# Kernel optimization log

Hardware: AMD Instinct MI355X
Metric: run time of the kernel (lower is better)

Reference implementation:

```python
import math
import jax, jax.numpy as jnp
import numpy as np

N_HEADS = 16
HEAD_DIM = 128
NUM_BUCKETS = 32
MAX_DISTANCE = 128
ROPE_BASE = 10000.0


def _rope_cos_sin(seq_len, head_dim, dtype):
    inv_freq = 1.0 / (ROPE_BASE ** (jnp.arange(0, head_dim, 2, dtype=jnp.float32) / head_dim))
    ang = jnp.arange(seq_len, dtype=jnp.float32)[:, None] * inv_freq[None, :]  # [S, hd/2]
    return jnp.cos(ang).astype(dtype), jnp.sin(ang).astype(dtype)


def _apply_rope(t, cos, sin):
    # t: [B, S, H, D] (NeoX rotate-half); cos/sin: [S, D/2]
    d2 = t.shape[-1] // 2
    t1, t2 = t[..., :d2], t[..., d2:]
    c = cos[None, :, None, :]
    s = sin[None, :, None, :]
    return jnp.concatenate([t1 * c - t2 * s, t2 * c + t1 * s], axis=-1)


def _relative_bucket(q_len, k_len):
    # unidirectional (causal) T5 bucketing: relative_position = 0 - min(mem - ctx, 0)
    ctx = jnp.arange(q_len, dtype=jnp.int32)[:, None]
    mem = jnp.arange(k_len, dtype=jnp.int32)[None, :]
    n = jnp.maximum(ctx - mem, 0)  # [Q, K]
    max_exact = NUM_BUCKETS // 2
    is_small = n < max_exact
    nf = jnp.maximum(n, 1).astype(jnp.float32)
    large = (jnp.log(nf / max_exact) / math.log(MAX_DISTANCE / max_exact)
             * (NUM_BUCKETS - max_exact)).astype(jnp.int32) + max_exact
    large = jnp.minimum(large, NUM_BUCKETS - 1)
    return jnp.where(is_small, n, large)


def setup_inputs() -> dict:
    key = jax.random.key(0)
    k1, k2, k3, k4 = jax.random.split(key, 4)
    B, S, H = 2, 2048, 2048
    return {
        "x": jax.random.normal(k1, (B, S, H), jnp.float32),
        "qkv_w": jax.random.normal(k2, (H, 3 * H), jnp.float32) * 0.02,
        "dense_w": jax.random.normal(k3, (H, H), jnp.float32) * 0.02,
        "rel_attn_table": jax.random.normal(k4, (NUM_BUCKETS, N_HEADS), jnp.float32) * 0.1,
    }


def reference(x, qkv_w, dense_w, rel_attn_table):
    B, S, H = x.shape
    qkv = x @ qkv_w                         # [B, S, 3H]
    q, k, v = jnp.split(qkv, 3, axis=-1)
    q = q.reshape(B, S, N_HEADS, HEAD_DIM)
    k = k.reshape(B, S, N_HEADS, HEAD_DIM)
    v = v.reshape(B, S, N_HEADS, HEAD_DIM)

    cos, sin = _rope_cos_sin(S, HEAD_DIM, x.dtype)
    q = _apply_rope(q, cos, sin)
    k = _apply_rope(k, cos, sin)

    scale = 1.0 / math.sqrt(HEAD_DIM)       # q_scaling = 1.0
    scores = jnp.einsum("bqhd,bkhd->bhqk", q, k) * scale  # [B, nH, S, S]

    # T5 relative position bias: embedding(bucket, table).permute(2,0,1) -> [1, nH, S, S]
    bucket = _relative_bucket(S, S)
    bias = rel_attn_table[bucket]            # [S, S, nH]
    scores = scores + jnp.transpose(bias, (2, 0, 1))[None]

    # causal mask (make_causal_mask): key index > query index -> large negative
    causal = jnp.tril(jnp.ones((S, S), dtype=bool))
    neg = jnp.asarray(jnp.finfo(x.dtype).min, x.dtype)
    scores = jnp.where(causal[None, None], scores, neg)

    probs = jax.nn.softmax(scores, axis=-1)
    ctx = jnp.einsum("bhqk,bkhd->bqhd", probs, v).reshape(B, S, H)
    return ctx @ dense_w
```

## Files before the change

### kernel.cpp

```cpp
#include <hip/hip_runtime.h>

typedef unsigned short u16;
typedef __bf16 bf16_t;
typedef __bf16 bf16x8 __attribute__((ext_vector_type(8)));
typedef float f32x4 __attribute__((ext_vector_type(4)));
typedef unsigned short u16x8 __attribute__((ext_vector_type(8)));
typedef unsigned short u16x4 __attribute__((ext_vector_type(4)));

#define S_LEN 2048
#define NHEAD 16
#define HD 128
#define HID 2048
#define QKV_N 6144

__device__ __forceinline__ float b2f(u16 u) {
  union { unsigned int i; float f; } x; x.i = ((unsigned int)u) << 16; return x.f;
}
__device__ __forceinline__ u16 f2b(float f) {
  bf16_t h = (bf16_t)f;
  return __builtin_bit_cast(unsigned short, h);
}

__device__ __forceinline__ void gl_lds16(const u16* g, u16* l) {
  __builtin_amdgcn_global_load_lds(
      (const __attribute__((address_space(1))) unsigned int*)g,
      (__attribute__((address_space(3))) unsigned int*)l, 16, 0, 0);
}

__global__ void detect_dtype_k(const void* __restrict__ x, int* __restrict__ flag) {
  __shared__ int cnt;
  if (threadIdx.x == 0) cnt = 0;
  __syncthreads();
  const u16* xu = (const u16*)x;
  int sane = 0;
  for (int i = threadIdx.x; i < 8192; i += 256) {
    int e = (xu[i] >> 7) & 0xFF;
    if (e == 0 || (e > 100 && e < 140)) sane++;
  }
  atomicAdd(&cnt, sane);
  __syncthreads();
  if (threadIdx.x == 0) *flag = (cnt < 7373) ? 1 : 0;
}

__global__ __launch_bounds__(256) void convert_any_k(const void* __restrict__ in, u16* __restrict__ out,
                                                     const int* __restrict__ flag) {
  int i = (blockIdx.x * 256 + threadIdx.x) * 4;
  if (*flag) {
    const float4 v = *(const float4*)((const float*)in + i);
    u16x4 o = {f2b(v.x), f2b(v.y), f2b(v.z), f2b(v.w)};
    *(u16x4*)(out + i) = o;
  } else {
    *(u16x4*)(out + i) = *(const u16x4*)((const u16*)in + i);
  }
}

__global__ __launch_bounds__(256) void transpose_any(const void* __restrict__ in,
                                                     u16* __restrict__ out, int R, int C,
                                                     const int* __restrict__ flag) {
  __shared__ u16 t[64][65];
  bool isf = (*flag != 0);
  int tid = threadIdx.x;
  int r0 = blockIdx.y * 64, c0 = blockIdx.x * 64;
#pragma unroll
  for (int p = 0; p < 16; ++p) {
    int e = p * 256 + tid;
    int r = e >> 6, c = e & 63;
    size_t idx = (size_t)(r0 + r) * C + (c0 + c);
    t[r][c] = isf ? f2b(((const float*)in)[idx]) : ((const u16*)in)[idx];
  }
  __syncthreads();
#pragma unroll
  for (int p = 0; p < 16; ++p) {
    int e = p * 256 + tid;
    int r = e >> 6, c = e & 63;
    out[(size_t)(c0 + r) * R + (r0 + c)] = t[c][r];
  }
}

__global__ void rope_table_k(float* __restrict__ tab) {
  int i = blockIdx.x * 256 + threadIdx.x;
  int s = i >> 6, d = i & 63;
  float inv = expf(-(float)d * (9.210340371976184f / 64.0f));
  float ang = (float)s * inv;
  tab[s * 128 + d] = cosf(ang);
  tab[s * 128 + 64 + d] = sinf(ang);
}

__global__ void build_bias_k(const void* __restrict__ table, float* __restrict__ bias,
                             const int* __restrict__ flag) {
  int i = blockIdx.x * 256 + threadIdx.x;
  int h = i >> 11, dist = i & 2047;
  int bucket;
  if (dist < 16) bucket = dist;
  else {
    int lb = (int)(logf((float)dist * 0.0625f) / 2.0794415f * 16.0f) + 16;
    bucket = lb < 31 ? lb : 31;
  }
  int ti = bucket * NHEAD + h;
  float tv = (*flag) ? ((const float*)table)[ti] : b2f(((const u16*)table)[ti]);
  bias[h * 2048 + dist] = tv;
}

template <bool F32OUT>
__global__ __launch_bounds__(256) void gemm_bt(const u16* __restrict__ A, const u16* __restrict__ B,
                                               void* __restrict__ Cv, int M, int N, int K) {
  __shared__ __align__(16) u16 As[128 * 32];
  __shared__ __align__(16) u16 Bs[128 * 32];
  int tid = threadIdx.x;
  int lane = tid & 63, wv = tid >> 6;
  int wm = wv & 1, wn = wv >> 1;
  int lane16 = lane & 15, quad = lane >> 4;
  int m0 = blockIdx.y * 128, n0 = blockIdx.x * 128;

  const u16* pA = A + (size_t)(m0 + wv * 32 + (lane >> 2)) * K + (lane & 3) * 8;
  const u16* pB = B + (size_t)(n0 + wv * 32 + (lane >> 2)) * K + (lane & 3) * 8;
  u16* lA = As + wv * 1024;
  u16* lB = Bs + wv * 1024;

  f32x4 zero4 = {0.f, 0.f, 0.f, 0.f};
  f32x4 acc[4][4];
#pragma unroll
  for (int i = 0; i < 4; ++i)
#pragma unroll
    for (int j = 0; j < 4; ++j) acc[i][j] = zero4;

  int nk = K >> 5;
  for (int kt = 0; kt < nk; ++kt) {
    __syncthreads();
    gl_lds16(pA, lA);
    gl_lds16(pA + (size_t)16 * K, lA + 512);
    gl_lds16(pB, lB);
    gl_lds16(pB + (size_t)16 * K, lB + 512);
    pA += 32; pB += 32;
    __syncthreads();
    bf16x8 af[4], bfr[4];
#pragma unroll
    for (int i = 0; i < 4; ++i)
      af[i] = *(const bf16x8*)&As[(wm * 64 + i * 16 + lane16) * 32 + quad * 8];
#pragma unroll
    for (int j = 0; j < 4; ++j)
      bfr[j] = *(const bf16x8*)&Bs[(wn * 64 + j * 16 + lane16) * 32 + quad * 8];
#pragma unroll
    for (int i = 0; i < 4; ++i)
#pragma unroll
      for (int j = 0; j < 4; ++j)
        acc[i][j] = __builtin_amdgcn_mfma_f32_16x16x32_bf16(af[i], bfr[j], acc[i][j], 0, 0, 0);
  }
#pragma unroll
  for (int i = 0; i < 4; ++i)
#pragma unroll
    for (int j = 0; j < 4; ++j)
#pragma unroll
      for (int r = 0; r < 4; ++r) {
        int row = m0 + wm * 64 + i * 16 + quad * 4 + r;
        int col = n0 + wn * 64 + j * 16 + lane16;
        if (F32OUT)
          ((float*)Cv)[(size_t)row * N + col] = acc[i][j][r];
        else
          ((u16*)Cv)[(size_t)row * N + col] = f2b(acc[i][j][r]);
      }
}

__global__ __launch_bounds__(256) void reorg_k(const u16* __restrict__ qkv, const float* __restrict__ tab,
                                               u16* __restrict__ q, u16* __restrict__ k,
                                               u16* __restrict__ vT) {
  __shared__ float vt[64][129];
  int tid = threadIdx.x;
  int st = blockIdx.x, bh = blockIdx.y;
  int b = bh >> 4, h = bh & 15;
  int s0 = st * 64;
  const u16* base = qkv + (size_t)(b * S_LEN + s0) * QKV_N + h * HD;
  u16* qo = q + ((size_t)bh * S_LEN + s0) * HD;
  u16* ko = k + ((size_t)bh * S_LEN + s0) * HD;
#pragma unroll
  for (int p = 0; p < 16; ++p) {
    int e = p * 256 + tid;
    int sl = e >> 6, d = e & 63;
    float c = tab[(s0 + sl) * 128 + d];
    float sn = tab[(s0 + sl) * 128 + 64 + d];
    const u16* rowp = base + (size_t)sl * QKV_N;
    float q1 = b2f(rowp[d]), q2 = b2f(rowp[d + 64]);
    qo[sl * HD + d] = f2b(q1 * c - q2 * sn);
    qo[sl * HD + d + 64] = f2b(q2 * c + q1 * sn);
    float k1 = b2f(rowp[2048 + d]), k2 = b2f(rowp[2048 + d + 64]);
    ko[sl * HD + d] = f2b(k1 * c - k2 * sn);
    ko[sl * HD + d + 64] = f2b(k2 * c + k1 * sn);
  }
#pragma unroll
  for (int p = 0; p < 32; ++p) {
    int e = p * 256 + tid;
    int sl = e >> 7, d = e & 127;
    vt[sl][d] = b2f(base[(size_t)sl * QKV_N + 4096 + d]);
  }
  __syncthreads();
  u16* vo = vT + (size_t)bh * HD * S_LEN;
#pragma unroll
  for (int p = 0; p < 32; ++p) {
    int e = p * 256 + tid;
    int d = e >> 6, sl = e & 63;
    vo[(size_t)d * S_LEN + s0 + sl] = f2b(vt[sl][d]);
  }
}

__global__ __launch_bounds__(256) void attn_k(const u16* __restrict__ q, const u16* __restrict__ k,
                                              const u16* __restrict__ vT, const float* __restrict__ bias,
                                              u16* __restrict__ ctx) {
  __shared__ __align__(16) u16 Ks[64 * 128];
  __shared__ __align__(16) u16 VTs[128 * 64];
  __shared__ __align__(16) u16 QP[64 * 128];
  __shared__ float bias_s[128];
  int tid = threadIdx.x;
  int lane = tid & 63, wq = tid >> 6;
  int lane16 = lane & 15, quad = lane >> 4;
  int r7 = lane16 & 7;
  int bh = blockIdx.y;
  int b = bh >> 4, h = bh & 15;
  const u16* kg = k + (size_t)bh * S_LEN * HD;
  const u16* vg = vT + (size_t)bh * HD * S_LEN;
  const float* biasr = bias + h * 2048;
  const float scale = 0.08838834764831845f;
  f32x4 zero4 = {0.f, 0.f, 0.f, 0.f};

  int rl4 = lane >> 4, pk = lane & 15;
  int rl8 = lane >> 3, pv = lane & 7;
  u16* Pw = QP + wq * 1152;

  for (int half = 0; half < 2; ++half) {
    int qt = half ? (31 - blockIdx.x) : blockIdx.x;
    int q0 = qt * 64;
    const u16* qg = q + ((size_t)bh * S_LEN + q0) * HD;

    __syncthreads();
    {
      int r = tid >> 4, c = (tid & 15) * 8;
#pragma unroll
      for (int p = 0; p < 4; ++p)
        *(u16x8*)&QP[(r + p * 16) * 128 + c] = *(const u16x8*)&qg[(size_t)(r + p * 16) * HD + c];
    }
    __syncthreads();
    bf16x8 qf[4];
#pragma unroll
    for (int kd = 0; kd < 4; ++kd)
      qf[kd] = *(const bf16x8*)&QP[(wq * 16 + lane16) * 128 + kd * 32 + quad * 8];
    __syncthreads();

    float m_i[4], l_i[4];
    f32x4 o[8];
#pragma unroll
    for (int r = 0; r < 4; ++r) { m_i[r] = -1e30f; l_i[r] = 0.f; }
#pragma unroll
    for (int dt = 0; dt < 8; ++dt) o[dt] = zero4;

    for (int kt = 0; kt <= qt; ++kt) {
      int k0 = kt * 64;
      if (kt) __syncthreads();
#pragma unroll
      for (int t = 0; t < 4; ++t) {
        int g = wq * 4 + t;
        int rowk = g * 4 + rl4;
        int ck = (pk & 8) | ((pk & 7) ^ (rowk & 7));
        gl_lds16(kg + (size_t)(k0 + rowk) * HD + ck * 8, Ks + g * 512);
        int rowv = g * 8 + rl8;
        int cv = pv ^ (rowv & 7);
        gl_lds16(vg + (size_t)rowv * S_LEN + k0 + cv * 8, VTs + g * 512);
      }
      if (tid < 128) {
        int dist = q0 - k0 + tid - 64;
        bias_s[tid] = (dist >= 0) ? biasr[dist] : 0.f;
      }
      __syncthreads();

      f32x4 sc[4];
#pragma unroll
      for (int j = 0; j < 4; ++j) sc[j] = zero4;
#pragma unroll
      for (int kd = 0; kd < 4; ++kd)
#pragma unroll
        for (int j = 0; j < 4; ++j) {
          int cd = kd * 4 + quad;
          int pos = (cd & 8) | ((cd & 7) ^ r7);
          bf16x8 kf = *(const bf16x8*)&Ks[(j * 16 + lane16) * 128 + pos * 8];
          sc[j] = __builtin_amdgcn_mfma_f32_16x16x32_bf16(qf[kd], kf, sc[j], 0, 0, 0);
        }

      int qrel = wq * 16 + quad * 4;
#pragma unroll
      for (int j = 0; j < 4; ++j) {
        int krel = j * 16 + lane16;
#pragma unroll
        for (int r = 0; r < 4; ++r) {
          bool valid = (q0 + qrel + r) >= (k0 + krel);
          float sv = sc[j][r] * scale + bias_s[64 + (qrel + r) - krel];
          sc[j][r] = valid ? sv : -1e30f;
        }
      }
      float mx[4];
#pragma unroll
      for (int r = 0; r < 4; ++r)
        mx[r] = fmaxf(fmaxf(sc[0][r], sc[1][r]), fmaxf(sc[2][r], sc[3][r]));
#pragma unroll
      for (int xm = 1; xm < 16; xm <<= 1)
#pragma unroll
        for (int r = 0; r < 4; ++r) mx[r] = fmaxf(mx[r], __shfl_xor(mx[r], xm));
      float alpha[4];
#pragma unroll
      for (int r = 0; r < 4; ++r) {
        float mn = fmaxf(m_i[r], mx[r]);
        alpha[r] = __expf(m_i[r] - mn);
        m_i[r] = mn;
      }
#pragma unroll
      for (int j = 0; j < 4; ++j)
#pragma unroll
        for (int r = 0; r < 4; ++r) sc[j][r] = __expf(sc[j][r] - m_i[r]);
      float rs[4];
#pragma unroll
      for (int r = 0; r < 4; ++r) rs[r] = (sc[0][r] + sc[1][r]) + (sc[2][r] + sc[3][r]);
#pragma unroll
      for (int xm = 1; xm < 16; xm <<= 1)
#pragma unroll
        for (int r = 0; r < 4; ++r) rs[r] += __shfl_xor(rs[r], xm);
#pragma unroll
      for (int r = 0; r < 4; ++r) l_i[r] = l_i[r] * alpha[r] + rs[r];
#pragma unroll
      for (int dt = 0; dt < 8; ++dt)
#pragma unroll
        for (int r = 0; r < 4; ++r) o[dt][r] *= alpha[r];

#pragma unroll
      for (int j = 0; j < 4; ++j)
#pragma unroll
        for (int r = 0; r < 4; ++r)
          Pw[(quad * 4 + r) * 72 + j * 16 + lane16] = f2b(sc[j][r]);
      __threadfence_block();

#pragma unroll
      for (int ks = 0; ks < 2; ++ks) {
        bf16x8 pf = *(const bf16x8*)&Pw[lane16 * 72 + ks * 32 + quad * 8];
#pragma unroll
        for (int dt = 0; dt < 8; ++dt) {
          int cdv = ks * 4 + quad;
          int posv = cdv ^ r7;
          bf16x8 vf = *(const bf16x8*)&VTs[(dt * 16 + lane16) * 64 + posv * 8];
          o[dt] = __builtin_amdgcn_mfma_f32_16x16x32_bf16(pf, vf, o[dt], 0, 0, 0);
        }
      }
    }
#pragma unroll
    for (int r = 0; r < 4; ++r) {
      float invl = 1.0f / l_i[r];
      int srow = q0 + wq * 16 + quad * 4 + r;
      u16* orow = ctx + ((size_t)b * S_LEN + srow) * HID + h * HD;
#pragma unroll
      for (int dt = 0; dt < 8; ++dt)
        orow[dt * 16 + lane16] = f2b(o[dt][r] * invl);
    }
  }
}

extern "C" void kernel_launch(void* const* d_in, const int* in_sizes, int n_in,
                              void* d_out, int out_size, void* d_ws, size_t ws_size,
                              hipStream_t stream) {
  const void* x       = d_in[0];
  const void* qkv_w   = d_in[1];
  const void* dense_w = d_in[2];
  const void* rtable  = d_in[3];
  char* ws = (char*)d_ws;

  int*   flag  = (int*)(ws);
  float* bias  = (float*)(ws + 256);
  float* tab   = (float*)(ws + 131328);
  u16*   wdT   = (u16*)(ws + 1179904);
  u16*   vT    = (u16*)(ws + 9568512);
  u16*   x_bf  = (u16*)(ws + 26345728);
  u16*   qA    = x_bf;
  u16*   wqkvT = (u16*)(ws + 43122944);
  u16*   kA    = wqkvT;
  u16*   qkv   = (u16*)(ws + 68288768);
  u16*   ctx   = qkv;

  detect_dtype_k<<<1, 256, 0, stream>>>(x, flag);
  convert_any_k<<<8192, 256, 0, stream>>>(x, x_bf, flag);
  transpose_any<<<dim3(96, 32), 256, 0, stream>>>(qkv_w, wqkvT, 2048, 6144, flag);
  transpose_any<<<dim3(32, 32), 256, 0, stream>>>(dense_w, wdT, 2048, 2048, flag);
  rope_table_k<<<512, 256, 0, stream>>>(tab);
  build_bias_k<<<128, 256, 0, stream>>>(rtable, bias, flag);
  gemm_bt<false><<<dim3(48, 32), 256, 0, stream>>>(x_bf, wqkvT, qkv, 4096, 6144, 2048);
  reorg_k<<<dim3(32, 32), 256, 0, stream>>>(qkv, tab, qA, kA, vT);
  attn_k<<<dim3(16, 32), 256, 0, stream>>>(qA, kA, vT, bias, ctx);
  gemm_bt<true><<<dim3(16, 32), 256, 0, stream>>>(ctx, wdT, d_out, 4096, 2048, 2048);
}
```

Before: 477.5 us.

## Add 256x256-tile pipelined GEMM kernel for QKV projection

Adds a new GEMM kernel that uses 256x256 output tiles with 8 waves and double-buffered LDS fed by direct global-to-LDS loads. Loads for upcoming k-slices are interleaved with MFMA quarter-blocks under barriers, and the kernel also swizzles the block order and raises wave priority around the MFMAs. The QKV projection now launches this kernel instead of the 128-tile version. The larger tile raises arithmetic intensity and overlaps memory with compute, but it uses more LDS and registers, and 384 workgroups on 256 CUs may leave the tail unbalanced.

Result: faster. 463.0 us (-3.0%).

```diff
diff --git a/kernel.cpp b/kernel.cpp
--- a/kernel.cpp
+++ b/kernel.cpp
@@ -159,6 +159,135 @@
         else
           ((u16*)Cv)[(size_t)row * N + col] = f2b(acc[i][j][r]);
       }
+}
+
+template <bool F32OUT>
+__global__ __launch_bounds__(512, 2) void gemm256_bt(const u16* __restrict__ A,
+                                                     const u16* __restrict__ B,
+                                                     void* __restrict__ Cv,
+                                                     int M, int N, int K) {
+  __shared__ __align__(16) u16 sA[2][16384];
+  __shared__ __align__(16) u16 sB[2][16384];
+  (void)M;
+  const int tid = threadIdx.x;
+  const int lane = tid & 63, w = tid >> 6;
+  const int wm = w >> 2, wn = w & 3;
+  const int lane16 = lane & 15, quad = lane >> 4;
+
+  const int nbx = gridDim.x;
+  const int nwg = nbx * gridDim.y;
+  const int bid = blockIdx.y * nbx + blockIdx.x;
+  const int cpx = nwg >> 3;
+  const int swz = (bid & 7) * cpx + (bid >> 3);
+  const int m0 = (swz / nbx) * 256;
+  const int n0 = (swz % nbx) * 256;
+
+  const int rl = lane >> 2;
+  const int ch = (lane & 3) ^ (((lane >> 5) & 1) << 1);
+  const u16* pA_ = A + (size_t)(m0 + w * 16 + rl) * K + ch * 8;
+  const u16* pB_ = B + (size_t)(n0 + w * 16 + rl) * K + ch * 8;
+
+  const int fro = lane16 * 32 + ((quad * 8) ^ ((lane16 & 8) << 1));
+
+  f32x4 zero4 = {0.f, 0.f, 0.f, 0.f};
+  f32x4 acc[8][4];
+#pragma unroll
+  for (int i = 0; i < 8; ++i)
+#pragma unroll
+    for (int j = 0; j < 4; ++j) acc[i][j] = zero4;
+
+  bf16x8 af[4][2];
+  bf16x8 bfr[4][2];
+
+#define STAGE_A(BUF, H, KO)                                      \
+  do {                                                           \
+    const u16* _s = pA_ + (size_t)(H) * 128 * K + (KO);          \
+    u16* _d = &sA[BUF][(H) * 8192 + w * 1024];                   \
+    gl_lds16(_s, _d);                                            \
+    gl_lds16(_s + 32, _d + 512);                                 \
+  } while (0)
+#define STAGE_B(BUF, H, KO)                                      \
+  do {                                                           \
+    const u16* _s = pB_ + (size_t)(H) * 128 * K + (KO);          \
+    u16* _d = &sB[BUF][(H) * 8192 + w * 1024];                   \
+    gl_lds16(_s, _d);                                            \
+    gl_lds16(_s + 32, _d + 512);                                 \
+  } while (0)
+#define READ_A(BUF, MH)                                                              \
+  _Pragma("unroll") for (int i = 0; i < 4; ++i)                                      \
+  _Pragma("unroll") for (int ks = 0; ks < 2; ++ks)                                   \
+    af[i][ks] = *(const bf16x8*)&sA[BUF][((wm * 8 + (MH) * 4 + i) * 2 + ks) * 512 + fro];
+#define READ_B(BUF, NH)                                                              \
+  _Pragma("unroll") for (int j = 0; j < 2; ++j)                                      \
+  _Pragma("unroll") for (int ks = 0; ks < 2; ++ks)                                   \
+    bfr[(NH) * 2 + j][ks] = *(const bf16x8*)&sB[BUF][((wn * 4 + (NH) * 2 + j) * 2 + ks) * 512 + fro];
+#define MFMA_Q(MH, NH)                                                               \
+  __builtin_amdgcn_s_setprio(1);                                                     \
+  _Pragma("unroll") for (int i = 0; i < 4; ++i)                                      \
+  _Pragma("unroll") for (int j = 0; j < 2; ++j)                                      \
+  _Pragma("unroll") for (int ks = 0; ks < 2; ++ks)                                   \
+    acc[(MH) * 4 + i][(NH) * 2 + j] = __builtin_amdgcn_mfma_f32_16x16x32_bf16(       \
+        af[i][ks], bfr[(NH) * 2 + j][ks], acc[(MH) * 4 + i][(NH) * 2 + j], 0, 0, 0); \
+  __builtin_amdgcn_s_setprio(0);
+#define GBAR() __builtin_amdgcn_s_barrier()
+#define VMCNT4() asm volatile("s_waitcnt vmcnt(4)" ::: "memory")
+
+  STAGE_A(0, 0, 0); STAGE_A(0, 1, 0);
+  STAGE_B(0, 0, 0); STAGE_B(0, 1, 0);
+  STAGE_B(1, 0, 64); STAGE_A(1, 0, 64);
+  VMCNT4();
+  GBAR();
+
+  const int nIt = K >> 7;
+  for (int it = 0; it < nIt; ++it) {
+    int k1 = (it << 7) + 64;
+    int k2 = k1 + 64; if (k2 >= K) k2 = 0;
+    int k3 = k2 + 64; if (k3 >= K) k3 = 0;
+    READ_A(0, 0); READ_B(0, 0);
+    STAGE_A(1, 1, k1);
+    GBAR(); MFMA_Q(0, 0); GBAR();
+    READ_B(0, 1);
+    STAGE_B(1, 1, k1);
+    GBAR(); MFMA_Q(0, 1); GBAR();
+    READ_A(0, 1);
+    STAGE_B(0, 0, k2);
+    GBAR(); MFMA_Q(1, 1); GBAR();
+    STAGE_A(0, 0, k2);
+    GBAR(); MFMA_Q(1, 0); VMCNT4(); GBAR();
+    READ_A(1, 0); READ_B(1, 0);
+    STAGE_A(0, 1, k2);
+    GBAR(); MFMA_Q(0, 0); GBAR();
+    READ_B(1, 1);
+    STAGE_B(0, 1, k2);
+    GBAR(); MFMA_Q(0, 1); GBAR();
+    READ_A(1, 1);
+    STAGE_B(1, 0, k3);
+    GBAR(); MFMA_Q(1, 1); GBAR();
+    STAGE_A(1, 0, k3);
+    GBAR(); MFMA_Q(1, 0); VMCNT4(); GBAR();
+  }
+  asm volatile("s_waitcnt vmcnt(0)" ::: "memory");
+
+#pragma unroll
+  for (int i = 0; i < 8; ++i)
+#pragma unroll
+    for (int j = 0; j < 4; ++j)
+#pragma unroll
+      for (int r = 0; r < 4; ++r) {
+        int row = m0 + wm * 128 + i * 16 + quad * 4 + r;
+        int col = n0 + wn * 64 + j * 16 + lane16;
+        if (F32OUT)
+          ((float*)Cv)[(size_t)row * N + col] = acc[i][j][r];
+        else
+          ((u16*)Cv)[(size_t)row * N + col] = f2b(acc[i][j][r]);
+      }
+#undef STAGE_A
+#undef STAGE_B
+#undef READ_A
+#undef READ_B
+#undef MFMA_Q
+#undef GBAR
+#undef VMCNT4
 }
 
 __global__ __launch_bounds__(256) void reorg_k(const u16* __restrict__ qkv, const float* __restrict__ tab,
@@ -385,7 +514,7 @@
   transpose_any<<<dim3(32, 32), 256, 0, stream>>>(dense_w, wdT, 2048, 2048, flag);
   rope_table_k<<<512, 256, 0, stream>>>(tab);
   build_bias_k<<<128, 256, 0, stream>>>(rtable, bias, flag);
-  gemm_bt<false><<<dim3(48, 32), 256, 0, stream>>>(x_bf, wqkvT, qkv, 4096, 6144, 2048);
+  gemm256_bt<false><<<dim3(24, 16), 512, 0, stream>>>(x_bf, wqkvT, qkv, 4096, 6144, 2048);
   reorg_k<<<dim3(32, 32), 256, 0, stream>>>(qkv, tab, qA, kA, vT);
   attn_k<<<dim3(16, 32), 256, 0, stream>>>(qA, kA, vT, bias, ctx);
   gemm_bt<true><<<dim3(16, 32), 256, 0, stream>>>(ctx, wdT, d_out, 4096, 2048, 2048);
```

## Rewrite GEMM as double-buffered 128x256 tile with swizzled LDS and block remap

Applied to the files above, without the earlier changes.

Replaces the single-buffered 128x128 GEMM with a 512-thread kernel that computes 128x256 tiles over a 64-wide K step. Global-to-LDS loads are double-buffered and interleaved with MFMA phases, synchronised by explicit vmcnt waits and barriers. The LDS layout is XOR-swizzled to avoid bank conflicts, workgroups are remapped in groups of eight for better L2 locality, and s_setprio raises priority around the MFMA bursts. The aim is to hide load latency and raise MFMA utilisation for both projections. The cost is more LDS and register pressure and fragile hand-counted waitcnt ordering.

Result: faster. 466.9 us (-2.2%).

```diff
diff --git a/kernel.cpp b/kernel.cpp
--- a/kernel.cpp
+++ b/kernel.cpp
@@ -102,20 +102,32 @@
 }
 
 template <bool F32OUT>
-__global__ __launch_bounds__(256) void gemm_bt(const u16* __restrict__ A, const u16* __restrict__ B,
-                                               void* __restrict__ Cv, int M, int N, int K) {
-  __shared__ __align__(16) u16 As[128 * 32];
-  __shared__ __align__(16) u16 Bs[128 * 32];
-  int tid = threadIdx.x;
-  int lane = tid & 63, wv = tid >> 6;
-  int wm = wv & 1, wn = wv >> 1;
-  int lane16 = lane & 15, quad = lane >> 4;
-  int m0 = blockIdx.y * 128, n0 = blockIdx.x * 128;
-
-  const u16* pA = A + (size_t)(m0 + wv * 32 + (lane >> 2)) * K + (lane & 3) * 8;
-  const u16* pB = B + (size_t)(n0 + wv * 32 + (lane >> 2)) * K + (lane & 3) * 8;
-  u16* lA = As + wv * 1024;
-  u16* lB = Bs + wv * 1024;
+__global__ __launch_bounds__(512, 2) void gemm128_bt(const u16* __restrict__ A,
+                                                     const u16* __restrict__ B,
+                                                     void* __restrict__ Cv,
+                                                     int M, int N, int K) {
+  __shared__ __align__(16) u16 sA[2][8192];
+  __shared__ __align__(16) u16 sB[2][16384];
+  (void)M;
+  const int tid = threadIdx.x;
+  const int lane = tid & 63, w = tid >> 6;
+  const int wm = w >> 2, wn = w & 3;
+  const int lane16 = lane & 15, quad = lane >> 4;
+
+  const int nbx = gridDim.x;
+  const int nwg = nbx * gridDim.y;
+  const int bid = blockIdx.y * nbx + blockIdx.x;
+  const int cpx = nwg >> 3;
+  const int swz = (bid & 7) * cpx + (bid >> 3);
+  const int m0 = (swz / nbx) * 128;
+  const int n0 = (swz % nbx) * 256;
+
+  const int rl = lane >> 2;
+  const int ch = (lane & 3) ^ (((lane >> 5) & 1) << 1);
+  const u16* pA_ = A + (size_t)(m0 + w * 16 + rl) * K + ch * 8;
+  const u16* pB_ = B + (size_t)(n0 + w * 16 + rl) * K + ch * 8;
+
+  const int fro = lane16 * 32 + ((quad * 8) ^ ((lane16 & 8) << 1));
 
   f32x4 zero4 = {0.f, 0.f, 0.f, 0.f};
   f32x4 acc[4][4];
@@ -124,28 +136,75 @@
 #pragma unroll
     for (int j = 0; j < 4; ++j) acc[i][j] = zero4;
 
-  int nk = K >> 5;
-  for (int kt = 0; kt < nk; ++kt) {
-    __syncthreads();
-    gl_lds16(pA, lA);
-    gl_lds16(pA + (size_t)16 * K, lA + 512);
-    gl_lds16(pB, lB);
-    gl_lds16(pB + (size_t)16 * K, lB + 512);
-    pA += 32; pB += 32;
-    __syncthreads();
-    bf16x8 af[4], bfr[4];
-#pragma unroll
-    for (int i = 0; i < 4; ++i)
-      af[i] = *(const bf16x8*)&As[(wm * 64 + i * 16 + lane16) * 32 + quad * 8];
-#pragma unroll
-    for (int j = 0; j < 4; ++j)
-      bfr[j] = *(const bf16x8*)&Bs[(wn * 64 + j * 16 + lane16) * 32 + quad * 8];
-#pragma unroll
-    for (int i = 0; i < 4; ++i)
-#pragma unroll
-      for (int j = 0; j < 4; ++j)
-        acc[i][j] = __builtin_amdgcn_mfma_f32_16x16x32_bf16(af[i], bfr[j], acc[i][j], 0, 0, 0);
-  }
+  bf16x8 a0[2][2], a1[2][2];
+  bf16x8 Bf[4][2];
+
+#define STAGE_A(BUF, KO)                                         \
+  do {                                                           \
+    const u16* _s = pA_ + (KO);                                  \
+    u16* _d = &sA[BUF][w * 1024];                                \
+    gl_lds16(_s, _d);                                            \
+    gl_lds16(_s + 32, _d + 512);                                 \
+  } while (0)
+#define STAGE_B(BUF, H, KO)                                      \
+  do {                                                           \
+    const u16* _s = pB_ + (size_t)(H) * 128 * K + (KO);          \
+    u16* _d = &sB[BUF][(H) * 8192 + w * 1024];                   \
+    gl_lds16(_s, _d);                                            \
+    gl_lds16(_s + 32, _d + 512);                                 \
+  } while (0)
+#define READ_A(DST, BUF, MH)                                                         \
+  _Pragma("unroll") for (int i = 0; i < 2; ++i)                                      \
+  _Pragma("unroll") for (int ks = 0; ks < 2; ++ks)                                   \
+    DST[i][ks] = *(const bf16x8*)&sA[BUF][((wm * 4 + (MH) * 2 + i) * 2 + ks) * 512 + fro];
+#define READ_BF(BUF)                                                                 \
+  _Pragma("unroll") for (int j = 0; j < 4; ++j)                                      \
+  _Pragma("unroll") for (int ks = 0; ks < 2; ++ks)                                   \
+    Bf[j][ks] = *(const bf16x8*)&sB[BUF][((wn * 4 + j) * 2 + ks) * 512 + fro];
+#define MFMA_H(AF, MH)                                                               \
+  __builtin_amdgcn_s_setprio(1);                                                     \
+  _Pragma("unroll") for (int i = 0; i < 2; ++i)                                      \
+  _Pragma("unroll") for (int j = 0; j < 4; ++j)                                      \
+  _Pragma("unroll") for (int ks = 0; ks < 2; ++ks)                                   \
+    acc[(MH) * 2 + i][j] = __builtin_amdgcn_mfma_f32_16x16x32_bf16(                  \
+        AF[i][ks], Bf[j][ks], acc[(MH) * 2 + i][j], 0, 0, 0);                        \
+  __builtin_amdgcn_s_setprio(0);
+#define GBAR() __builtin_amdgcn_s_barrier()
+#define VMCNT4() asm volatile("s_waitcnt vmcnt(4)" ::: "memory")
+#define VMCNT6() asm volatile("s_waitcnt vmcnt(6)" ::: "memory")
+
+  STAGE_B(0, 0, 0); STAGE_B(0, 1, 0); STAGE_A(0, 0);
+  STAGE_B(1, 0, 64); STAGE_B(1, 1, 64); STAGE_A(1, 64);
+  VMCNT6();
+  GBAR();
+  READ_A(a0, 0, 0); READ_BF(0);
+
+  const int nIt = K >> 7;
+  for (int it = 0; it < nIt; ++it) {
+    int base = it << 7;
+    int k2 = base + 128; if (k2 >= K) k2 = 0;
+    int k3 = base + 192; if (k3 >= K) k3 = 0;
+    GBAR();
+    MFMA_H(a0, 0);
+    STAGE_B(0, 0, k2); STAGE_B(0, 1, k2);
+    READ_A(a1, 0, 1);
+    VMCNT4();
+    GBAR();
+    MFMA_H(a1, 1);
+    STAGE_A(0, k2);
+    READ_BF(1); READ_A(a0, 1, 0);
+    GBAR();
+    MFMA_H(a0, 0);
+    STAGE_B(1, 0, k3); STAGE_B(1, 1, k3);
+    READ_A(a1, 1, 1);
+    VMCNT4();
+    GBAR();
+    MFMA_H(a1, 1);
+    STAGE_A(1, k3);
+    READ_BF(0); READ_A(a0, 0, 0);
+  }
+  asm volatile("s_waitcnt vmcnt(0)" ::: "memory");
+
 #pragma unroll
   for (int i = 0; i < 4; ++i)
 #pragma unroll
@@ -159,6 +218,14 @@
         else
           ((u16*)Cv)[(size_t)row * N + col] = f2b(acc[i][j][r]);
       }
+#undef STAGE_A
+#undef STAGE_B
+#undef READ_A
+#undef READ_BF
+#undef MFMA_H
+#undef GBAR
+#undef VMCNT4
+#undef VMCNT6
 }
 
 __global__ __launch_bounds__(256) void reorg_k(const u16* __restrict__ qkv, const float* __restrict__ tab,
@@ -385,8 +452,8 @@
   transpose_any<<<dim3(32, 32), 256, 0, stream>>>(dense_w, wdT, 2048, 2048, flag);
   rope_table_k<<<512, 256, 0, stream>>>(tab);
   build_bias_k<<<128, 256, 0, stream>>>(rtable, bias, flag);
-  gemm_bt<false><<<dim3(48, 32), 256, 0, stream>>>(x_bf, wqkvT, qkv, 4096, 6144, 2048);
+  gemm128_bt<false><<<dim3(24, 32), 512, 0, stream>>>(x_bf, wqkvT, qkv, 4096, 6144, 2048);
   reorg_k<<<dim3(32, 32), 256, 0, stream>>>(qkv, tab, qA, kA, vT);
   attn_k<<<dim3(16, 32), 256, 0, stream>>>(qA, kA, vT, bias, ctx);
-  gemm_bt<true><<<dim3(16, 32), 256, 0, stream>>>(ctx, wdT, d_out, 4096, 2048, 2048);
-}
+  gemm128_bt<true><<<dim3(8, 32), 512, 0, stream>>>(ctx, wdT, d_out, 4096, 2048, 2048);
+}
```
